# Kernel optimization log

Hardware: AMD Instinct MI355X
Metric: run time of the kernel (lower is better)

## Reference

```python
import jax, jax.numpy as jnp
import numpy as np

WIN = (9, 9, 9)
EPS = 1e-05


def setup_inputs() -> dict:
    key = jax.random.key(0)
    k1, k2 = jax.random.split(key)
    shape = (2, 1, 160, 160, 160)  # [B, C=1, D, H, W]
    x = jax.random.normal(k1, shape, dtype=jnp.float32)
    y = jax.random.normal(k2, shape, dtype=jnp.float32)
    return {"x": x, "y": y}


def _convn(z, kernel):
    # dense 3D box-sum conv, VALID (inputs are pre-padded), NCDHW layout
    return jax.lax.conv_general_dilated(
        z, kernel, window_strides=(1, 1, 1), padding='VALID',
        dimension_numbers=('NCDHW', 'OIDHW', 'NCDHW'))


def reference(x, y):
    p = tuple(w // 2 for w in WIN)  # (4, 4, 4)
    pad_cfg = ((0, 0), (0, 0), (p[0], p[0]), (p[1], p[1]), (p[2], p[2]))
    kernel = jnp.ones((1, 1) + WIN, dtype=x.dtype)

    x_pad = jnp.pad(x, pad_cfg, mode='edge')      # replicate padding
    y_pad = jnp.pad(y, pad_cfg, mode='edge')
    ones_pad = jnp.pad(jnp.ones_like(x), pad_cfg, mode='edge')

    N = _convn(ones_pad, kernel)                  # local window counts (all = 729 here)
    xm = _convn(x_pad, kernel) / N                # local mean of x
    ym = _convn(y_pad, kernel) / N                # local mean of y
    x2 = _convn(x_pad * x_pad, kernel) / N        # local E[x^2]
    y2 = _convn(y_pad * y_pad, kernel) / N        # local E[y^2]
    xy = _convn(x_pad * y_pad, kernel) / N        # local E[xy]

    cross = xy - xm * ym
    var_x = x2 - xm * xm
    var_y = y2 - ym * ym
    ncc = cross * cross / (var_x * var_y + EPS)
    return -jnp.mean(ncc)
```

## Files before the change

kernel.cpp:

```cpp
#include <hip/hip_runtime.h>

#define DIM 160
#define SLICE (DIM * DIM)
#define TH 16
#define TW 16
#define CD 40

#define SIDX(c,i,j) ((c)*680 + (i)*28 + (j))
#define TIDX(c,i,j) ((c)*456 + (i)*28 + (j))
#define UIDX(c,i,j) ((c)*260 + (i)*16 + (j))

__global__ __launch_bounds__(256, 4)
void lncc_kernel(const float* __restrict__ x, const float* __restrict__ y,
                 float* __restrict__ out)
{
    __shared__ __align__(16) float S[5 * 680];
    __shared__ __align__(16) float T[5 * 456];
    __shared__ __align__(16) float U[5 * 260];
    __shared__ float wsum[4];

    const int t  = threadIdx.x;
    const int w0 = blockIdx.x * TW;
    const int h0 = blockIdx.y * TH;
    const int bz = blockIdx.z;
    const int b   = bz >> 2;
    const int zo0 = (bz & 3) * CD;

    const float* xb = x + (size_t)b * (DIM * SLICE);
    const float* yb = y + (size_t)b * (DIM * SLICE);

    const int h1  = t / 6;
    const int w41 = t - h1 * 6;
    const int gh  = min(max(h0 - 4 + h1, 0), DIM - 1);
    const int gwb = w0 - 4 + 4 * w41;
    const bool fast = (gwb >= 0) && (gwb + 3 < DIM);
    const int jc0 = min(max(gwb + 0, 0), DIM - 1);
    const int jc1 = min(max(gwb + 1, 0), DIM - 1);
    const int jc2 = min(max(gwb + 2, 0), DIM - 1);
    const int jc3 = min(max(gwb + 3, 0), DIM - 1);

    auto load4 = [&](const float* sl) -> float4 {
        const float* row = sl + (size_t)gh * DIM;
        if (fast) return *reinterpret_cast<const float4*>(row + gwb);
        float4 r;
        r.x = row[jc0]; r.y = row[jc1]; r.z = row[jc2]; r.w = row[jc3];
        return r;
    };

    const int c2  = t / 24;
    const int r2  = t - c2 * 24;
    const int w42 = r2 >> 2;
    const int i02 = (r2 & 3) * 4;

    const int i3 = t >> 2;
    const int j3 = (t & 3) * 4;

    const int i4 = t >> 4;
    const int j4 = t & 15;

    float hist[9][5];
    float rs[5] = {0.f, 0.f, 0.f, 0.f, 0.f};
    float acc = 0.f;

    float4 xv = {0,0,0,0}, yv = {0,0,0,0};
    {
        const int z0 = min(max(zo0 - 4, 0), DIM - 1);
        if (t < 144) {
            xv = load4(xb + (size_t)z0 * SLICE);
            yv = load4(yb + (size_t)z0 * SLICE);
        }
    }

    const int zlast = zo0 + CD + 3;
    for (int base = zo0 - 4; base <= zlast; base += 9) {
        #pragma unroll
        for (int p = 0; p < 9; ++p) {
            const int zi = base + p;
            if (zi <= zlast) {
                if (t < 144) {
                    const int jw = 4 * w41;
                    *reinterpret_cast<float4*>(&S[SIDX(0, h1, jw)]) = xv;
                    *reinterpret_cast<float4*>(&S[SIDX(1, h1, jw)]) = yv;
                    *reinterpret_cast<float4*>(&S[SIDX(2, h1, jw)]) = xv * xv;
                    *reinterpret_cast<float4*>(&S[SIDX(3, h1, jw)]) = yv * yv;
                    *reinterpret_cast<float4*>(&S[SIDX(4, h1, jw)]) = xv * yv;
                }
                __syncthreads();

                if (t < 144 && zi < zlast) {
                    const int zn = min(max(zi + 1, 0), DIM - 1);
                    xv = load4(xb + (size_t)zn * SLICE);
                    yv = load4(yb + (size_t)zn * SLICE);
                }

                if (t < 120) {
                    const int jw = 4 * w42;
                    float4 s = {0,0,0,0};
                    #pragma unroll
                    for (int k = 0; k < 9; ++k)
                        s += *reinterpret_cast<const float4*>(&S[SIDX(c2, i02 + k, jw)]);
                    *reinterpret_cast<float4*>(&T[TIDX(c2, i02, jw)]) = s;
                    #pragma unroll
                    for (int m = 1; m < 4; ++m) {
                        s += *reinterpret_cast<const float4*>(&S[SIDX(c2, i02 + 8 + m, jw)])
                           - *reinterpret_cast<const float4*>(&S[SIDX(c2, i02 + m - 1, jw)]);
                        *reinterpret_cast<float4*>(&T[TIDX(c2, i02 + m, jw)]) = s;
                    }
                }
                __syncthreads();

                if (t < 64) {
                    #pragma unroll
                    for (int c = 0; c < 5; ++c) {
                        const float4 t0 = *reinterpret_cast<const float4*>(&T[TIDX(c, i3, j3)]);
                        const float4 t1 = *reinterpret_cast<const float4*>(&T[TIDX(c, i3, j3 + 4)]);
                        const float4 t2 = *reinterpret_cast<const float4*>(&T[TIDX(c, i3, j3 + 8)]);
                        float4 uo;
                        float s = t0.x + t0.y + t0.z + t0.w
                                + t1.x + t1.y + t1.z + t1.w + t2.x;
                        uo.x = s;
                        s += t2.y - t0.x; uo.y = s;
                        s += t2.z - t0.y; uo.z = s;
                        s += t2.w - t0.z; uo.w = s;
                        *reinterpret_cast<float4*>(&U[UIDX(c, i3, j3)]) = uo;
                    }
                }
                __syncthreads();

                float u[5];
                #pragma unroll
                for (int c = 0; c < 5; ++c) {
                    u[c] = U[UIDX(c, i4, j4)];
                    rs[c] += u[c];
                    hist[p][c] = u[c];
                }
                if (zi >= zo0 + 4) {
                    const float inv = 1.0f / 729.0f;
                    const float xm = rs[0] * inv, ym = rs[1] * inv;
                    const float x2 = rs[2] * inv, y2 = rs[3] * inv;
                    const float xy = rs[4] * inv;
                    const float cross = xy - xm * ym;
                    const float vx = x2 - xm * xm;
                    const float vy = y2 - ym * ym;
                    acc += cross * cross / (vx * vy + 1e-5f);
                    const int po = (p + 1) % 9;
                    #pragma unroll
                    for (int c = 0; c < 5; ++c)
                        rs[c] -= hist[po][c];
                }
            }
        }
    }

    #pragma unroll
    for (int off = 32; off > 0; off >>= 1)
        acc += __shfl_down(acc, off, 64);
    const int wave = t >> 6;
    if ((t & 63) == 0) wsum[wave] = acc;
    __syncthreads();
    if (t == 0) {
        const float s = wsum[0] + wsum[1] + wsum[2] + wsum[3];
        atomicAdd(out, -s * (1.0f / 8192000.0f));
    }
}

extern "C" void kernel_launch(void* const* d_in, const int* in_sizes, int n_in,
                              void* d_out, int out_size, void* d_ws, size_t ws_size,
                              hipStream_t stream)
{
    const float* x = (const float*)d_in[0];
    const float* y = (const float*)d_in[1];
    float* out = (float*)d_out;

    hipMemsetAsync(out, 0, sizeof(float), stream);

    dim3 grid(DIM / TW, DIM / TH, 2 * (DIM / CD));
    lncc_kernel<<<grid, 256, 0, stream>>>(x, y, out);
}
```

Before: 163.5 us.

## Fuse W-direction box sum into load stage, dropping one LDS pass and barrier

Threads 160-255 now each load a 12-wide row segment of x and y into registers and compute the W-direction 9-tap running sums for all five products before writing to shared memory. This removes the raw staging buffer and one shared-memory pass, so each slice needs two barriers instead of three. Work is split by warp role: the load/W-sum threads are separate from the 80 threads doing the H-direction pass. The cost is more registers (double-buffered 12-element arrays), which lowers launch bounds to 3 blocks per SM. Overlapping global loads are also redundant by 12/4.

```diff
diff --git a/kernel.cpp b/kernel.cpp
--- a/kernel.cpp
+++ b/kernel.cpp
@@ -5,18 +5,17 @@
 #define TH 16
 #define TW 16
 #define CD 40
+#define WSTR 20
+#define WPL (24 * WSTR)
+#define USTR 20
+#define UPL (16 * USTR)
 
-#define SIDX(c,i,j) ((c)*680 + (i)*28 + (j))
-#define TIDX(c,i,j) ((c)*456 + (i)*28 + (j))
-#define UIDX(c,i,j) ((c)*260 + (i)*16 + (j))
-
-__global__ __launch_bounds__(256, 4)
+__global__ __launch_bounds__(256, 3)
 void lncc_kernel(const float* __restrict__ x, const float* __restrict__ y,
                  float* __restrict__ out)
 {
-    __shared__ __align__(16) float S[5 * 680];
-    __shared__ __align__(16) float T[5 * 456];
-    __shared__ __align__(16) float U[5 * 260];
+    __shared__ __align__(16) float Wb[5 * WPL];
+    __shared__ __align__(16) float Ub[5 * UPL];
     __shared__ float wsum[4];
 
     const int t  = threadIdx.x;
@@ -29,47 +28,48 @@
     const float* xb = x + (size_t)b * (DIM * SLICE);
     const float* yb = y + (size_t)b * (DIM * SLICE);
 
-    const int h1  = t / 6;
-    const int w41 = t - h1 * 6;
-    const int gh  = min(max(h0 - 4 + h1, 0), DIM - 1);
-    const int gwb = w0 - 4 + 4 * w41;
-    const bool fast = (gwb >= 0) && (gwb + 3 < DIM);
-    const int jc0 = min(max(gwb + 0, 0), DIM - 1);
-    const int jc1 = min(max(gwb + 1, 0), DIM - 1);
-    const int jc2 = min(max(gwb + 2, 0), DIM - 1);
-    const int jc3 = min(max(gwb + 3, 0), DIM - 1);
+    const bool isA = t >= 160;
+    const int at = t - 160;
+    const int rA = at >> 2;
+    const int qA = at & 3;
+    const int ghA = min(max(h0 - 4 + rA, 0), DIM - 1);
+    const int jlA = w0 - 4 + 4 * qA;
+    const bool fastA = (jlA >= 0) && (jlA + 11 < DIM);
 
-    auto load4 = [&](const float* sl) -> float4 {
-        const float* row = sl + (size_t)gh * DIM;
-        if (fast) return *reinterpret_cast<const float4*>(row + gwb);
-        float4 r;
-        r.x = row[jc0]; r.y = row[jc1]; r.z = row[jc2]; r.w = row[jc3];
-        return r;
-    };
-
-    const int c2  = t / 24;
-    const int r2  = t - c2 * 24;
-    const int w42 = r2 >> 2;
-    const int i02 = (r2 & 3) * 4;
-
-    const int i3 = t >> 2;
-    const int j3 = (t & 3) * 4;
+    const int cB = t >> 4;
+    const int rB = t & 15;
+    const int wB = (rB >> 2) * 4;
+    const int iB = (rB & 3) * 4;
 
     const int i4 = t >> 4;
     const int j4 = t & 15;
 
+    float cx[12], cy[12], nx[12], ny[12];
     float hist[9][5];
     float rs[5] = {0.f, 0.f, 0.f, 0.f, 0.f};
     float acc = 0.f;
 
-    float4 xv = {0,0,0,0}, yv = {0,0,0,0};
-    {
-        const int z0 = min(max(zo0 - 4, 0), DIM - 1);
-        if (t < 144) {
-            xv = load4(xb + (size_t)z0 * SLICE);
-            yv = load4(yb + (size_t)z0 * SLICE);
+    auto loadA = [&](int z, float* vx, float* vy) {
+        const float* rx = xb + (size_t)z * SLICE + (size_t)ghA * DIM;
+        const float* ry = yb + (size_t)z * SLICE + (size_t)ghA * DIM;
+        if (fastA) {
+            #pragma unroll
+            for (int g = 0; g < 3; ++g) {
+                const float4 a = *reinterpret_cast<const float4*>(rx + jlA + 4 * g);
+                const float4 c = *reinterpret_cast<const float4*>(ry + jlA + 4 * g);
+                vx[4*g+0] = a.x; vx[4*g+1] = a.y; vx[4*g+2] = a.z; vx[4*g+3] = a.w;
+                vy[4*g+0] = c.x; vy[4*g+1] = c.y; vy[4*g+2] = c.z; vy[4*g+3] = c.w;
+            }
+        } else {
+            #pragma unroll
+            for (int m = 0; m < 12; ++m) {
+                const int jj = min(max(jlA + m, 0), DIM - 1);
+                vx[m] = rx[jj]; vy[m] = ry[jj];
+            }
         }
-    }
+    };
+
+    if (isA) loadA(min(max(zo0 - 4, 0), DIM - 1), cx, cy);
 
     const int zlast = zo0 + CD + 3;
     for (int base = zo0 - 4; base <= zlast; base += 9) {
@@ -77,76 +77,71 @@
         for (int p = 0; p < 9; ++p) {
             const int zi = base + p;
             if (zi <= zlast) {
-                if (t < 144) {
-                    const int jw = 4 * w41;
-                    *reinterpret_cast<float4*>(&S[SIDX(0, h1, jw)]) = xv;
-                    *reinterpret_cast<float4*>(&S[SIDX(1, h1, jw)]) = yv;
-                    *reinterpret_cast<float4*>(&S[SIDX(2, h1, jw)]) = xv * xv;
-                    *reinterpret_cast<float4*>(&S[SIDX(3, h1, jw)]) = yv * yv;
-                    *reinterpret_cast<float4*>(&S[SIDX(4, h1, jw)]) = xv * yv;
-                }
-                __syncthreads();
-
-                if (t < 144 && zi < zlast) {
-                    const int zn = min(max(zi + 1, 0), DIM - 1);
-                    xv = load4(xb + (size_t)zn * SLICE);
-                    yv = load4(yb + (size_t)zn * SLICE);
-                }
-
-                if (t < 120) {
-                    const int jw = 4 * w42;
-                    float4 s = {0,0,0,0};
+                if (isA) {
+                    if (zi < zlast) loadA(min(max(zi + 1, 0), DIM - 1), nx, ny);
                     #pragma unroll
-                    for (int k = 0; k < 9; ++k)
-                        s += *reinterpret_cast<const float4*>(&S[SIDX(c2, i02 + k, jw)]);
-                    *reinterpret_cast<float4*>(&T[TIDX(c2, i02, jw)]) = s;
-                    #pragma unroll
-                    for (int m = 1; m < 4; ++m) {
-                        s += *reinterpret_cast<const float4*>(&S[SIDX(c2, i02 + 8 + m, jw)])
-                           - *reinterpret_cast<const float4*>(&S[SIDX(c2, i02 + m - 1, jw)]);
-                        *reinterpret_cast<float4*>(&T[TIDX(c2, i02 + m, jw)]) = s;
+                    for (int c = 0; c < 5; ++c) {
+                        float pr[12];
+                        #pragma unroll
+                        for (int m = 0; m < 12; ++m)
+                            pr[m] = (c == 0) ? cx[m]
+                                  : (c == 1) ? cy[m]
+                                  : (c == 2) ? cx[m] * cx[m]
+                                  : (c == 3) ? cy[m] * cy[m]
+                                             : cx[m] * cy[m];
+                        float s = pr[0]+pr[1]+pr[2]+pr[3]+pr[4]
+                                + pr[5]+pr[6]+pr[7]+pr[8];
+                        float4 o;
+                        o.x = s;
+                        s += pr[9]  - pr[0]; o.y = s;
+                        s += pr[10] - pr[1]; o.z = s;
+                        s += pr[11] - pr[2]; o.w = s;
+                        *reinterpret_cast<float4*>(
+                            &Wb[c * WPL + rA * WSTR + 4 * qA]) = o;
                     }
                 }
                 __syncthreads();
 
-                if (t < 64) {
+                if (t < 80) {
+                    float4 s = {0,0,0,0};
                     #pragma unroll
-                    for (int c = 0; c < 5; ++c) {
-                        const float4 t0 = *reinterpret_cast<const float4*>(&T[TIDX(c, i3, j3)]);
-                        const float4 t1 = *reinterpret_cast<const float4*>(&T[TIDX(c, i3, j3 + 4)]);
-                        const float4 t2 = *reinterpret_cast<const float4*>(&T[TIDX(c, i3, j3 + 8)]);
-                        float4 uo;
-                        float s = t0.x + t0.y + t0.z + t0.w
-                                + t1.x + t1.y + t1.z + t1.w + t2.x;
-                        uo.x = s;
-                        s += t2.y - t0.x; uo.y = s;
-                        s += t2.z - t0.y; uo.z = s;
-                        s += t2.w - t0.z; uo.w = s;
-                        *reinterpret_cast<float4*>(&U[UIDX(c, i3, j3)]) = uo;
+                    for (int k = 0; k < 9; ++k)
+                        s += *reinterpret_cast<const float4*>(
+                                 &Wb[cB*WPL + (iB + k)*WSTR + wB]);
+                    *reinterpret_cast<float4*>(&Ub[cB*UPL + iB*USTR + wB]) = s;
+                    #pragma unroll
+                    for (int m = 1; m < 4; ++m) {
+                        s += *reinterpret_cast<const float4*>(
+                                 &Wb[cB*WPL + (iB + 8 + m)*WSTR + wB])
+                           - *reinterpret_cast<const float4*>(
+                                 &Wb[cB*WPL + (iB + m - 1)*WSTR + wB]);
+                        *reinterpret_cast<float4*>(
+                            &Ub[cB*UPL + (iB + m)*USTR + wB]) = s;
                     }
                 }
                 __syncthreads();
 
-                float u[5];
                 #pragma unroll
                 for (int c = 0; c < 5; ++c) {
-                    u[c] = U[UIDX(c, i4, j4)];
-                    rs[c] += u[c];
-                    hist[p][c] = u[c];
+                    const float u = Ub[c*UPL + i4*USTR + j4];
+                    rs[c] += u;
+                    hist[p][c] = u;
                 }
                 if (zi >= zo0 + 4) {
                     const float inv = 1.0f / 729.0f;
-                    const float xm = rs[0] * inv, ym = rs[1] * inv;
-                    const float x2 = rs[2] * inv, y2 = rs[3] * inv;
-                    const float xy = rs[4] * inv;
-                    const float cross = xy - xm * ym;
-                    const float vx = x2 - xm * xm;
-                    const float vy = y2 - ym * ym;
-                    acc += cross * cross / (vx * vy + 1e-5f);
+                    const float xm = rs[0]*inv, ym = rs[1]*inv;
+                    const float x2 = rs[2]*inv, y2 = rs[3]*inv, xy = rs[4]*inv;
+                    const float cross = xy - xm*ym;
+                    const float vx_ = x2 - xm*xm;
+                    const float vy_ = y2 - ym*ym;
+                    acc += cross*cross / (vx_*vy_ + 1e-5f);
                     const int po = (p + 1) % 9;
                     #pragma unroll
-                    for (int c = 0; c < 5; ++c)
-                        rs[c] -= hist[po][c];
+                    for (int c = 0; c < 5; ++c) rs[c] -= hist[po][c];
+                }
+                if (isA && zi < zlast) {
+                    #pragma unroll
+                    for (int m = 0; m < 12; ++m) { cx[m] = nx[m]; cy[m] = ny[m]; }
                 }
             }
         }
```

Result: slower. 213.3 us (+30.5%).
